# Kernel tuning notes

Hardware: AMD Instinct MI355X
Metric: run time of the kernel (lower is better)

Reference implementation:

```python
import jax, jax.numpy as jnp
from jax import lax
import numpy as np

CONF_THRES = 0.25
IOU_THRES = 0.45
MAX_WH = 7680.0   # per-class box offset (yolov5 agnostic=False trick)
TOP_K = 5000      # pre-NMS candidate cap (yolov5 uses max_nms=30000; capped for tractable IoU matrix)


def _xywh2xyxy(b):
    xy, wh = b[..., :2], b[..., 2:4]
    half = wh * 0.5
    return jnp.concatenate([xy - half, xy + half], axis=-1)


def _box_iou(a, b):
    # a: [K,4], b: [K,4] xyxy -> [K,K]
    area_a = (a[:, 2] - a[:, 0]) * (a[:, 3] - a[:, 1])
    area_b = (b[:, 2] - b[:, 0]) * (b[:, 3] - b[:, 1])
    lt = jnp.maximum(a[:, None, :2], b[None, :, :2])
    rb = jnp.minimum(a[:, None, 2:], b[None, :, 2:])
    wh = jnp.clip(rb - lt, 0.0)
    inter = wh[..., 0] * wh[..., 1]
    return inter / (area_a[:, None] + area_b[None, :] - inter + 1e-7)


def _nms_single(pred_i, max_det):
    # pred_i: [N, 5+nc] = (x, y, w, h, obj, cls...)
    obj = pred_i[:, 4]
    cls_conf = pred_i[:, 5:] * obj[:, None]          # conf = obj * cls
    score = jnp.max(cls_conf, axis=-1)                # best class (multi_label=False)
    cls = jnp.argmax(cls_conf, axis=-1).astype(pred_i.dtype)
    boxes = _xywh2xyxy(pred_i[:, :4])
    valid = (obj > CONF_THRES) & (score > CONF_THRES)
    mscore = jnp.where(valid, score, -1.0)

    # pre-NMS top-k candidates by confidence (yolov5 sorts by conf)
    top_s, idx = lax.top_k(mscore, TOP_K)
    tb = boxes[idx]                                   # [K,4]
    tc = cls[idx]                                     # [K]
    tvalid = top_s > 0.0

    # offset boxes by class so different classes never suppress each other
    ob = tb + (tc * MAX_WH)[:, None]
    iou = lax.stop_gradient(_box_iou(ob, ob))         # [K,K]
    ar = jnp.arange(TOP_K)

    def step(keep, i):
        sup = keep[i] & (iou[i] > IOU_THRES) & (ar > i)
        return keep & ~sup, None

    keep, _ = lax.scan(step, tvalid, ar)
    keep = keep & tvalid

    fscore = jnp.where(keep, top_s, -1.0)
    fs, fi = lax.top_k(fscore, max_det)
    det = jnp.concatenate([tb[fi], top_s[fi][:, None], tc[fi][:, None]], axis=-1)  # [max_det, 6]
    return jnp.where((fs > 0.0)[:, None], det, 0.0)


def setup_inputs() -> dict:
    key = jax.random.key(0)
    k1, k2, k3, k4 = jax.random.split(key, 4)
    B, N, NC = 8, 25200, 80
    xy = jax.random.uniform(k1, (B, N, 2)) * 608.0 + 16.0
    wh = jax.random.uniform(k2, (B, N, 2)) * 120.0 + 8.0
    obj = jax.random.uniform(k3, (B, N, 1))
    cls = jax.random.uniform(k4, (B, N, NC))
    pred = jnp.concatenate([xy, wh, obj, cls], axis=-1).astype(jnp.float32)
    return {"pred": pred, "max_det": 300}


def reference(pred, max_det):
    # pred: [B, N, 5+nc] -> detections [B, max_det, 6] = (x1, y1, x2, y2, conf, cls)
    return jax.vmap(lambda p: _nms_single(p, max_det))(pred)
```

## Files before the change

kernel.cpp:

```cpp
#include <hip/hip_runtime.h>

typedef unsigned long long ull;

#define N_PRED 25200
#define NCLS   80
#define ROWW   85
#define TOPK   5000
#define IOU_T  0.45f
#define MAXWH  7680.0f

#define K2T    1024
#define MAXE   25
#define CAP    512
#define CAPB   256
#define PTPB   256
#define PROWS  128
#define K4T    1024
#define MAXE4  5
#define SELN   320

__device__ __forceinline__ int SIX(int d) { return d + (d >> 5); }

__device__ __forceinline__ void scan_find(const unsigned* hist, int nb, unsigned k, ull* sbd) {
  const int l = (int)threadIdx.x;
  const int bpl = nb >> 6;
  unsigned s = 0;
  for (int j = 0; j < bpl; ++j) s += hist[SIX(l * bpl + j)];
  unsigned suf = s;
  #pragma unroll
  for (int o = 1; o < 64; o <<= 1) {
    unsigned t = __shfl_down(suf, (unsigned)o, 64);
    if (l + o < 64) suf += t;
  }
  unsigned sufN = __shfl_down(suf, 1u, 64);
  if (l == 63) sufN = 0;
  if (suf >= k && sufN < k) {
    unsigned cum = sufN;
    for (int j = bpl - 1; j >= 0; --j) {
      unsigned c = hist[SIX(l * bpl + j)];
      if (cum + c >= k) { sbd[0] = (ull)(l * bpl + j); sbd[1] = (ull)(k - cum); break; }
      cum += c;
    }
  }
}

__global__ __launch_bounds__(1024) void zero_kernel(unsigned* __restrict__ z, int nwords) {
  int i = blockIdx.x * 1024 + (int)threadIdx.x;
  if (i < nwords) z[i] = 0u;
}

__global__ __launch_bounds__(PTPB) void prep_kernel(const float* __restrict__ pred,
    ull* __restrict__ pk, unsigned char* __restrict__ cls8, unsigned* __restrict__ ghist) {
  __shared__ float sr[PROWS * ROWW];
  __shared__ unsigned hist[2048];
  const int b = blockIdx.y;
  const int rbase = blockIdx.x * PROWS;
  int nrows = N_PRED - rbase; if (nrows > PROWS) nrows = PROWS;
  const int tid = (int)threadIdx.x;
  for (int i = tid; i < 2048; i += PTPB) hist[i] = 0;
  const float* src = pred + ((size_t)b * N_PRED + rbase) * ROWW;
  const int nfl4 = (nrows * ROWW) >> 2;
  for (int i = tid; i < nfl4; i += PTPB) {
    float4 t; __builtin_memcpy(&t, src + i * 4, 16);
    *(float4*)&sr[i * 4] = t;
  }
  __syncthreads();
  const int r = tid >> 1, h = tid & 1;
  if (r < nrows) {
    const float* row = sr + r * ROWW;
    float obj = row[4];
    float best = -1.0f; int bi = 0;
    const int c0 = h * 40;
    for (int c = 0; c < 40; ++c) {
      float p = __fmul_rn(row[5 + c0 + c], obj);
      if (p > best) { best = p; bi = c0 + c; }
    }
    float ob_ = __shfl_xor(best, 1, 64);
    int   oi  = __shfl_xor(bi, 1, 64);
    if (h == 0) {
      if (!(best >= ob_)) { best = ob_; bi = oi; }
      bool valid = (obj > 0.25f) && (best > 0.25f);
      float ms = valid ? best : -1.0f;
      unsigned kb = __float_as_uint(ms);
      kb = (kb & 0x80000000u) ? ~kb : (kb | 0x80000000u);
      const int g = rbase + r;
      pk[(size_t)b * N_PRED + g] = ((ull)kb << 32) | (unsigned)~(unsigned)g;
      cls8[(size_t)b * N_PRED + g] = (unsigned char)bi;
      atomicAdd(&hist[kb >> 21], 1u);
    }
  }
  __syncthreads();
  for (int i = tid; i < 2048; i += PTPB) {
    unsigned cn = hist[i];
    if (cn) atomicAdd(&ghist[b * 2048 + i], cn);
  }
}

__global__ __launch_bounds__(K2T) void thresh_kernel(const ull* __restrict__ pkArr,
    const unsigned* __restrict__ ghist, const unsigned char* __restrict__ cls8,
    ull* __restrict__ bucket, unsigned* __restrict__ bucketCnt) {
  __shared__ unsigned hist[2112];
  __shared__ ull sbd[2];
  const int b = blockIdx.x;
  const int tid = (int)threadIdx.x;
  ull v[MAXE];
  #pragma unroll
  for (int e = 0; e < MAXE; ++e) {
    int i = tid + e * K2T;
    v[e] = (i < N_PRED) ? pkArr[(size_t)b * N_PRED + i] : 0ull;
  }
  unsigned k = TOPK;
  ull pfx = 0;
  for (int i = tid; i < 2048; i += K2T) hist[SIX(i)] = ghist[b * 2048 + i];
  __syncthreads();
  if (tid < 64) scan_find(hist, 2048, k, sbd);
  __syncthreads();
  {
    ull d = sbd[0]; unsigned kp = (unsigned)sbd[1];
    unsigned c = hist[SIX((int)d)];
    pfx |= d << 53; k = kp;
    if (kp != c) {
      const int shifts[5] = {42, 31, 20, 9, 0};
      const int widths[5] = {11, 11, 11, 11, 9};
      for (int p = 0; p < 5; ++p) {
        const int sh = shifts[p];
        const int nb = 1 << widths[p];
        __syncthreads();
        for (int i = tid; i < 2112; i += K2T) hist[i] = 0;
        __syncthreads();
        const int hb = sh + widths[p];
        const ull hm = ~((1ull << hb) - 1ull);
        #pragma unroll
        for (int e = 0; e < MAXE; ++e) {
          ull pv = v[e];
          if ((pv & hm) == pfx)
            atomicAdd(&hist[SIX((int)((pv >> sh) & (ull)(nb - 1)))], 1u);
        }
        __syncthreads();
        if (tid < 64) scan_find(hist, nb, k, sbd);
        __syncthreads();
        ull d2 = sbd[0]; unsigned kp2 = (unsigned)sbd[1];
        unsigned c2 = hist[SIX((int)d2)];
        pfx |= d2 << sh; k = kp2;
        if (kp2 == c2) break;
      }
    }
  }
  const ull thr = pfx;
  #pragma unroll
  for (int e = 0; e < MAXE; ++e) {
    ull pv = v[e];
    if (pv >= thr && (pv >> 63)) {
      unsigned idx = ~(unsigned)(pv & 0xFFFFFFFFull);
      int c = (int)cls8[(size_t)b * N_PRED + idx];
      unsigned pos = atomicAdd(&bucketCnt[b * NCLS + c], 1u);
      if (pos < CAP) bucket[((size_t)b * NCLS + c) * CAP + pos] = pv;
    }
  }
}

__global__ __launch_bounds__(64) void nms_kernel(const ull* __restrict__ bucket,
    const unsigned* __restrict__ bucketCnt, const float* __restrict__ pred,
    ull* __restrict__ keptPk, float4* __restrict__ keptBox, float2* __restrict__ keptSC,
    unsigned* __restrict__ keptCnt) {
  const int c = blockIdx.x, b = blockIdx.y, lane = (int)threadIdx.x;
  __shared__ ull su[CAPB];
  __shared__ ull spk[CAPB];
  __shared__ float4 sob[CAPB];
  __shared__ float4 srb[CAPB];
  unsigned kxu = bucketCnt[b * NCLS + c];
  int kx = (kxu > CAPB) ? CAPB : (int)kxu;
  if (kx == 0) return;
  const float cf = (float)c;
  const float off = __fmul_rn(cf, MAXWH);
  const ull* bk = bucket + ((size_t)b * NCLS + c) * CAP;
  for (int i = lane; i < kx; i += 64) su[i] = bk[i];
  __syncthreads();
  {
    ull mine[4]; int rk[4] = {0, 0, 0, 0};
    #pragma unroll
    for (int r = 0; r < 4; ++r) mine[r] = (r * 64 + lane < kx) ? su[r * 64 + lane] : 0ull;
    for (int j = 0; j < kx; ++j) {
      ull x = su[j];
      #pragma unroll
      for (int r = 0; r < 4; ++r) rk[r] += (x > mine[r]) ? 1 : 0;
    }
    #pragma unroll
    for (int r = 0; r < 4; ++r)
      if (r * 64 + lane < kx) spk[rk[r]] = mine[r];
  }
  __syncthreads();
  for (int i = lane; i < kx; i += 64) {
    unsigned idx = ~(unsigned)(spk[i] & 0xFFFFFFFFull);
    float4 t0; __builtin_memcpy(&t0, pred + ((size_t)b * N_PRED + idx) * ROWW, 16);
    float hw = __fmul_rn(t0.z, 0.5f), hh = __fmul_rn(t0.w, 0.5f);
    float4 rb = make_float4(__fsub_rn(t0.x, hw), __fsub_rn(t0.y, hh),
                            __fadd_rn(t0.x, hw), __fadd_rn(t0.y, hh));
    srb[i] = rb;
    sob[i] = make_float4(__fadd_rn(rb.x, off), __fadd_rn(rb.y, off),
                         __fadd_rn(rb.z, off), __fadd_rn(rb.w, off));
  }
  __syncthreads();
  ull rowm[4][4] = {{0ull}};
  #pragma unroll
  for (int r = 0; r < 4; ++r) {
    if (r * 64 < kx) {
      const int i = r * 64 + lane;
      const bool act = i < kx;
      float4 A = sob[act ? i : 0];
      float areaA = __fmul_rn(__fsub_rn(A.z, A.x), __fsub_rn(A.w, A.y));
      #pragma unroll
      for (int w = 0; w < 4; ++w) {
        if (w >= r && w * 64 < kx) {
          ull m = 0ull;
          int jmax = kx - w * 64; if (jmax > 64) jmax = 64;
          for (int jj = 0; jj < jmax; ++jj) {
            const int j = w * 64 + jj;
            float4 Bx = sob[j];
            float areaB = __fmul_rn(__fsub_rn(Bx.z, Bx.x), __fsub_rn(Bx.w, Bx.y));
            float wx = fmaxf(__fsub_rn(fminf(A.z, Bx.z), fmaxf(A.x, Bx.x)), 0.0f);
            float wy = fmaxf(__fsub_rn(fminf(A.w, Bx.w), fmaxf(A.y, Bx.y)), 0.0f);
            float inter = __fmul_rn(wx, wy);
            float denom = __fadd_rn(__fsub_rn(__fadd_rn(areaA, areaB), inter), 1e-7f);
            float iou = __fdiv_rn(inter, denom);
            if (act && j > i && iou > IOU_T) m |= 1ull << jj;
          }
          rowm[r][w] = m;
        }
      }
    }
  }
  ull alive[4];
  #pragma unroll
  for (int w = 0; w < 4; ++w) {
    int rem = kx - w * 64;
    alive[w] = (rem >= 64) ? ~0ull : (rem > 0 ? ((1ull << rem) - 1ull) : 0ull);
  }
  #pragma unroll
  for (int w = 0; w < 4; ++w) {
    if (w * 64 < kx) {
      int bmax = kx - w * 64; if (bmax > 64) bmax = 64;
      for (int bit = 0; bit < bmax; ++bit) {
        if ((alive[w] >> bit) & 1ull) {
          #pragma unroll
          for (int w2 = 0; w2 < 4; ++w2) {
            if (w2 >= w && w2 * 64 < kx) {
              ull row = __shfl(rowm[w][w2], bit, 64);
              alive[w2] &= ~row;
            }
          }
        }
      }
    }
  }
  int tot = 0;
  #pragma unroll
  for (int w = 0; w < 4; ++w) tot += (int)__popcll(alive[w]);
  unsigned gbase = 0;
  if (lane == 0) gbase = atomicAdd(&keptCnt[b], (unsigned)tot);
  gbase = __shfl(gbase, 0, 64);
  unsigned pre = 0;
  #pragma unroll
  for (int w = 0; w < 4; ++w) {
    if (w * 64 < kx) {
      ull aw = alive[w];
      int i = w * 64 + lane;
      bool kp = (i < kx) && ((aw >> lane) & 1ull);
      if (kp) {
        unsigned pos = gbase + pre + (unsigned)__popcll(aw & ((1ull << lane) - 1ull));
        if (pos < TOPK) {
          ull p = spk[i];
          keptPk[(size_t)b * TOPK + pos] = p;
          keptBox[(size_t)b * TOPK + pos] = srb[i];
          keptSC[(size_t)b * TOPK + pos] =
              make_float2(__uint_as_float((unsigned)(p >> 32) & 0x7FFFFFFFu), cf);
        }
      }
      pre += (unsigned)__popcll(aw);
    }
  }
}

__global__ __launch_bounds__(K4T) void out_kernel(const ull* __restrict__ keptPk,
    const float4* __restrict__ keptBox, const float2* __restrict__ keptSC,
    const unsigned* __restrict__ keptCnt, float* __restrict__ out, int maxdet) {
  __shared__ unsigned hist[2112];
  __shared__ ull sbd[2];
  __shared__ ull sPk[SELN];
  __shared__ int sSlot[SELN];
  __shared__ unsigned scnt;
  const int b = blockIdx.x;
  const int tid = (int)threadIdx.x;
  float* ob = out + (size_t)b * maxdet * 6;
  const unsigned K = keptCnt[b];
  const unsigned kk = (K < (unsigned)maxdet) ? K : (unsigned)maxdet;
  for (int i = (int)kk * 6 + tid; i < maxdet * 6; i += K4T) ob[i] = 0.0f;
  if (kk == 0) return;
  ull v[MAXE4];
  #pragma unroll
  for (int e = 0; e < MAXE4; ++e) {
    unsigned i = (unsigned)tid + e * K4T;
    v[e] = (i < K) ? keptPk[(size_t)b * TOPK + i] : 0ull;
  }
  ull thr = 1ull;
  if (K > (unsigned)maxdet) {
    unsigned k = kk;
    ull pfx = 0;
    const int shifts[6] = {53, 42, 31, 20, 9, 0};
    const int widths[6] = {11, 11, 11, 11, 11, 9};
    for (int p = 0; p < 6; ++p) {
      const int sh = shifts[p];
      const int nb = 1 << widths[p];
      for (int i = tid; i < 2112; i += K4T) hist[i] = 0;
      __syncthreads();
      const int hb = sh + widths[p];
      const ull hm = (hb >= 64) ? 0ull : ~((1ull << hb) - 1ull);
      #pragma unroll
      for (int e = 0; e < MAXE4; ++e) {
        ull pv = v[e];
        if (pv != 0ull && (pv & hm) == pfx)
          atomicAdd(&hist[SIX((int)((pv >> sh) & (ull)(nb - 1)))], 1u);
      }
      __syncthreads();
      if (tid < 64) scan_find(hist, nb, k, sbd);
      __syncthreads();
      ull d = sbd[0]; unsigned kp = (unsigned)sbd[1];
      unsigned c = hist[SIX((int)d)];
      pfx |= d << sh; k = kp;
      if (kp == c) break;
      __syncthreads();
    }
    thr = pfx;
  }
  if (tid == 0) scnt = 0;
  __syncthreads();
  const int lane = tid & 63;
  #pragma unroll
  for (int e = 0; e < MAXE4; ++e) {
    unsigned i = (unsigned)tid + e * K4T;
    bool sel = (i < K) && (v[e] >= thr);
    ull m = __ballot(sel);
    if (m) {
      unsigned basep = 0;
      if (lane == 0) basep = atomicAdd(&scnt, (unsigned)__popcll(m));
      basep = __shfl(basep, 0, 64);
      if (sel) {
        unsigned pos = basep + (unsigned)__popcll(m & ((1ull << lane) - 1ull));
        if (pos < SELN) { sPk[pos] = v[e]; sSlot[pos] = (int)i; }
      }
    }
  }
  __syncthreads();
  const int n = (int)scnt;
  for (int i = tid; i < n; i += K4T) {
    ull mypk = sPk[i];
    int rank = 0;
    for (int j = 0; j < n; ++j) rank += (sPk[j] > mypk) ? 1 : 0;
    if (rank < maxdet) {
      int slot = sSlot[i];
      float4 bx = keptBox[(size_t)b * TOPK + slot];
      float2 sc = keptSC[(size_t)b * TOPK + slot];
      float* dst = ob + (size_t)rank * 6;
      dst[0] = bx.x; dst[1] = bx.y; dst[2] = bx.z; dst[3] = bx.w;
      dst[4] = sc.x; dst[5] = sc.y;
    }
  }
}

extern "C" void kernel_launch(void* const* d_in, const int* in_sizes, int n_in,
                              void* d_out, int out_size, void* d_ws, size_t ws_size,
                              hipStream_t stream) {
  const float* pred = (const float*)d_in[0];
  const int B = in_sizes[0] / (N_PRED * ROWW);
  const int maxdet = out_size / (B * 6);

  char* p = (char*)d_ws;
  auto carve = [&](size_t bytes) { char* r = p; p += (bytes + 255) & ~(size_t)255; return (void*)r; };
  ull*           pk   = (ull*)carve((size_t)B * N_PRED * 8);
  unsigned char* cls8 = (unsigned char*)carve((size_t)B * N_PRED);
  size_t zbytes = (size_t)B * 2048 * 4 + (size_t)B * NCLS * 4 + (size_t)B * 4;
  char*     zbase     = (char*)carve(zbytes);
  unsigned* ghist     = (unsigned*)zbase;
  unsigned* bucketCnt = (unsigned*)(zbase + (size_t)B * 2048 * 4);
  unsigned* keptCnt   = (unsigned*)(zbase + (size_t)B * 2048 * 4 + (size_t)B * NCLS * 4);
  ull*      bucket  = (ull*)carve((size_t)B * NCLS * CAP * 8);
  ull*      keptPk  = (ull*)carve((size_t)B * TOPK * 8);
  float4*   keptBox = (float4*)carve((size_t)B * TOPK * 16);
  float2*   keptSC  = (float2*)carve((size_t)B * TOPK * 8);

  const int nwords = (int)(zbytes / 4);
  zero_kernel<<<(nwords + 1023) / 1024, 1024, 0, stream>>>((unsigned*)zbase, nwords);
  prep_kernel<<<dim3((N_PRED + PROWS - 1) / PROWS, B), PTPB, 0, stream>>>(pred, pk, cls8, ghist);
  thresh_kernel<<<B, K2T, 0, stream>>>(pk, ghist, cls8, bucket, bucketCnt);
  nms_kernel<<<dim3(NCLS, B), 64, 0, stream>>>(bucket, bucketCnt, pred,
                                               keptPk, keptBox, keptSC, keptCnt);
  out_kernel<<<B, K4T, 0, stream>>>(keptPk, keptBox, keptSC, keptCnt, (float*)d_out, maxdet);
}
```

Before: 111.9 us.

## Fuse threshold, per-class NMS and output selection into one per-batch kernel

Merges the threshold/bucketing, per-class NMS and final top-k output kernels into a single 1024-thread block per batch. Each wavefront handles classes in turn, with the per-class bucket cap reduced to 128. The prep kernel now processes one row per loop step across a whole wavefront, reading the row directly from global memory and reducing the class max with shuffles instead of staging rows in LDS. This removes two launches and global counter traffic. The cost is that NMS parallelism drops from 640 blocks to 8 blocks of 16 wavefronts, and the smaller cap risks dropping candidates in large classes.

```diff
diff --git a/kernel.cpp b/kernel.cpp
--- a/kernel.cpp
+++ b/kernel.cpp
@@ -9,13 +9,9 @@
 #define IOU_T  0.45f
 #define MAXWH  7680.0f
 
-#define K2T    1024
 #define MAXE   25
-#define CAP    512
-#define CAPB   256
-#define PTPB   256
-#define PROWS  128
-#define K4T    1024
+#define CAP    128
+#define PRPB   256
 #define MAXE4  5
 #define SELN   320
 
@@ -49,69 +45,79 @@
   if (i < nwords) z[i] = 0u;
 }
 
-__global__ __launch_bounds__(PTPB) void prep_kernel(const float* __restrict__ pred,
+__global__ __launch_bounds__(256) void prep_kernel(const float* __restrict__ pred,
     ull* __restrict__ pk, unsigned char* __restrict__ cls8, unsigned* __restrict__ ghist) {
-  __shared__ float sr[PROWS * ROWW];
   __shared__ unsigned hist[2048];
   const int b = blockIdx.y;
-  const int rbase = blockIdx.x * PROWS;
-  int nrows = N_PRED - rbase; if (nrows > PROWS) nrows = PROWS;
-  const int tid = (int)threadIdx.x;
-  for (int i = tid; i < 2048; i += PTPB) hist[i] = 0;
-  const float* src = pred + ((size_t)b * N_PRED + rbase) * ROWW;
-  const int nfl4 = (nrows * ROWW) >> 2;
-  for (int i = tid; i < nfl4; i += PTPB) {
-    float4 t; __builtin_memcpy(&t, src + i * 4, 16);
-    *(float4*)&sr[i * 4] = t;
-  }
-  __syncthreads();
-  const int r = tid >> 1, h = tid & 1;
-  if (r < nrows) {
-    const float* row = sr + r * ROWW;
+  const int tid = (int)threadIdx.x, lane = tid & 63, wv = tid >> 6;
+  for (int i = tid; i < 2048; i += 256) hist[i] = 0;
+  __syncthreads();
+  const int rbase = blockIdx.x * PRPB + wv * 64;
+  int rows = N_PRED - rbase; if (rows > 64) rows = 64;
+  ull mypk = 0; int mycls = 0, mybin = 0;
+  #pragma unroll 4
+  for (int t = 0; t < rows; ++t) {
+    const float* row = pred + ((size_t)b * N_PRED + (rbase + t)) * ROWW;
     float obj = row[4];
-    float best = -1.0f; int bi = 0;
-    const int c0 = h * 40;
-    for (int c = 0; c < 40; ++c) {
-      float p = __fmul_rn(row[5 + c0 + c], obj);
-      if (p > best) { best = p; bi = c0 + c; }
-    }
-    float ob_ = __shfl_xor(best, 1, 64);
-    int   oi  = __shfl_xor(bi, 1, 64);
-    if (h == 0) {
-      if (!(best >= ob_)) { best = ob_; bi = oi; }
+    float best = __fmul_rn(row[5 + lane], obj);
+    int bi = lane;
+    if (lane < 16) {
+      float p2 = __fmul_rn(row[69 + lane], obj);
+      if (p2 > best) { best = p2; bi = 64 + lane; }
+    }
+    #pragma unroll
+    for (int m = 32; m; m >>= 1) {
+      float ob = __shfl_xor(best, m, 64);
+      int   oi = __shfl_xor(bi, m, 64);
+      if (ob > best || (ob == best && oi < bi)) { best = ob; bi = oi; }
+    }
+    if (lane == t) {
       bool valid = (obj > 0.25f) && (best > 0.25f);
       float ms = valid ? best : -1.0f;
       unsigned kb = __float_as_uint(ms);
       kb = (kb & 0x80000000u) ? ~kb : (kb | 0x80000000u);
-      const int g = rbase + r;
-      pk[(size_t)b * N_PRED + g] = ((ull)kb << 32) | (unsigned)~(unsigned)g;
-      cls8[(size_t)b * N_PRED + g] = (unsigned char)bi;
-      atomicAdd(&hist[kb >> 21], 1u);
-    }
-  }
-  __syncthreads();
-  for (int i = tid; i < 2048; i += PTPB) {
+      mypk = ((ull)kb << 32) | (unsigned)~(unsigned)(rbase + t);
+      mycls = bi; mybin = (int)(kb >> 21);
+    }
+  }
+  if (lane < rows) {
+    const int g = rbase + lane;
+    pk[(size_t)b * N_PRED + g] = mypk;
+    cls8[(size_t)b * N_PRED + g] = (unsigned char)mycls;
+    atomicAdd(&hist[mybin], 1u);
+  }
+  __syncthreads();
+  for (int i = tid; i < 2048; i += 256) {
     unsigned cn = hist[i];
     if (cn) atomicAdd(&ghist[b * 2048 + i], cn);
   }
 }
 
-__global__ __launch_bounds__(K2T) void thresh_kernel(const ull* __restrict__ pkArr,
+__global__ __launch_bounds__(1024) void snms_kernel(const ull* __restrict__ pkArr,
     const unsigned* __restrict__ ghist, const unsigned char* __restrict__ cls8,
-    ull* __restrict__ bucket, unsigned* __restrict__ bucketCnt) {
+    const float* __restrict__ pred, ull* __restrict__ bucket,
+    ull* __restrict__ keptPk, float4* __restrict__ keptBox, float2* __restrict__ keptSC,
+    float* __restrict__ out, int maxdet) {
   __shared__ unsigned hist[2112];
   __shared__ ull sbd[2];
+  __shared__ unsigned bCnt[NCLS];
+  __shared__ unsigned keptCnt;
+  __shared__ unsigned scnt;
+  __shared__ ull wscr[16 * 384];
   const int b = blockIdx.x;
-  const int tid = (int)threadIdx.x;
+  const int tid = (int)threadIdx.x, lane = tid & 63, wv = tid >> 6;
+
+  if (tid < NCLS) bCnt[tid] = 0;
+  if (tid == 0) { keptCnt = 0; scnt = 0; }
   ull v[MAXE];
   #pragma unroll
   for (int e = 0; e < MAXE; ++e) {
-    int i = tid + e * K2T;
+    int i = tid + e * 1024;
     v[e] = (i < N_PRED) ? pkArr[(size_t)b * N_PRED + i] : 0ull;
   }
   unsigned k = TOPK;
   ull pfx = 0;
-  for (int i = tid; i < 2048; i += K2T) hist[SIX(i)] = ghist[b * 2048 + i];
+  for (int i = tid; i < 2048; i += 1024) hist[SIX(i)] = ghist[b * 2048 + i];
   __syncthreads();
   if (tid < 64) scan_find(hist, 2048, k, sbd);
   __syncthreads();
@@ -126,7 +132,7 @@
         const int sh = shifts[p];
         const int nb = 1 << widths[p];
         __syncthreads();
-        for (int i = tid; i < 2112; i += K2T) hist[i] = 0;
+        for (int i = tid; i < 2112; i += 1024) hist[i] = 0;
         __syncthreads();
         const int hb = sh + widths[p];
         const ull hm = ~((1ull << hb) - 1ull);
@@ -153,192 +159,176 @@
     if (pv >= thr && (pv >> 63)) {
       unsigned idx = ~(unsigned)(pv & 0xFFFFFFFFull);
       int c = (int)cls8[(size_t)b * N_PRED + idx];
-      unsigned pos = atomicAdd(&bucketCnt[b * NCLS + c], 1u);
+      unsigned pos = atomicAdd(&bCnt[c], 1u);
       if (pos < CAP) bucket[((size_t)b * NCLS + c) * CAP + pos] = pv;
     }
   }
-}
-
-__global__ __launch_bounds__(64) void nms_kernel(const ull* __restrict__ bucket,
-    const unsigned* __restrict__ bucketCnt, const float* __restrict__ pred,
-    ull* __restrict__ keptPk, float4* __restrict__ keptBox, float2* __restrict__ keptSC,
-    unsigned* __restrict__ keptCnt) {
-  const int c = blockIdx.x, b = blockIdx.y, lane = (int)threadIdx.x;
-  __shared__ ull su[CAPB];
-  __shared__ ull spk[CAPB];
-  __shared__ float4 sob[CAPB];
-  __shared__ float4 srb[CAPB];
-  unsigned kxu = bucketCnt[b * NCLS + c];
-  int kx = (kxu > CAPB) ? CAPB : (int)kxu;
-  if (kx == 0) return;
-  const float cf = (float)c;
-  const float off = __fmul_rn(cf, MAXWH);
-  const ull* bk = bucket + ((size_t)b * NCLS + c) * CAP;
-  for (int i = lane; i < kx; i += 64) su[i] = bk[i];
-  __syncthreads();
-  {
-    ull mine[4]; int rk[4] = {0, 0, 0, 0};
-    #pragma unroll
-    for (int r = 0; r < 4; ++r) mine[r] = (r * 64 + lane < kx) ? su[r * 64 + lane] : 0ull;
-    for (int j = 0; j < kx; ++j) {
-      ull x = su[j];
-      #pragma unroll
-      for (int r = 0; r < 4; ++r) rk[r] += (x > mine[r]) ? 1 : 0;
-    }
-    #pragma unroll
-    for (int r = 0; r < 4; ++r)
-      if (r * 64 + lane < kx) spk[rk[r]] = mine[r];
-  }
-  __syncthreads();
-  for (int i = lane; i < kx; i += 64) {
-    unsigned idx = ~(unsigned)(spk[i] & 0xFFFFFFFFull);
-    float4 t0; __builtin_memcpy(&t0, pred + ((size_t)b * N_PRED + idx) * ROWW, 16);
-    float hw = __fmul_rn(t0.z, 0.5f), hh = __fmul_rn(t0.w, 0.5f);
-    float4 rb = make_float4(__fsub_rn(t0.x, hw), __fsub_rn(t0.y, hh),
-                            __fadd_rn(t0.x, hw), __fadd_rn(t0.y, hh));
-    srb[i] = rb;
-    sob[i] = make_float4(__fadd_rn(rb.x, off), __fadd_rn(rb.y, off),
-                         __fadd_rn(rb.z, off), __fadd_rn(rb.w, off));
-  }
-  __syncthreads();
-  ull rowm[4][4] = {{0ull}};
-  #pragma unroll
-  for (int r = 0; r < 4; ++r) {
-    if (r * 64 < kx) {
-      const int i = r * 64 + lane;
-      const bool act = i < kx;
-      float4 A = sob[act ? i : 0];
-      float areaA = __fmul_rn(__fsub_rn(A.z, A.x), __fsub_rn(A.w, A.y));
-      #pragma unroll
-      for (int w = 0; w < 4; ++w) {
-        if (w >= r && w * 64 < kx) {
-          ull m = 0ull;
-          int jmax = kx - w * 64; if (jmax > 64) jmax = 64;
-          for (int jj = 0; jj < jmax; ++jj) {
-            const int j = w * 64 + jj;
-            float4 Bx = sob[j];
-            float areaB = __fmul_rn(__fsub_rn(Bx.z, Bx.x), __fsub_rn(Bx.w, Bx.y));
-            float wx = fmaxf(__fsub_rn(fminf(A.z, Bx.z), fmaxf(A.x, Bx.x)), 0.0f);
-            float wy = fmaxf(__fsub_rn(fminf(A.w, Bx.w), fmaxf(A.y, Bx.y)), 0.0f);
-            float inter = __fmul_rn(wx, wy);
-            float denom = __fadd_rn(__fsub_rn(__fadd_rn(areaA, areaB), inter), 1e-7f);
-            float iou = __fdiv_rn(inter, denom);
-            if (act && j > i && iou > IOU_T) m |= 1ull << jj;
-          }
-          rowm[r][w] = m;
+  __syncthreads();
+
+  ull* skey = wscr + (size_t)wv * 384;
+  float4* sow = (float4*)(skey + 128);
+  for (int cc = wv; cc < NCLS; cc += 16) {
+    unsigned kxu = bCnt[cc];
+    int kx = (kxu > (unsigned)CAP) ? CAP : (int)kxu;
+    if (kx == 0) continue;
+    const float cf = (float)cc;
+    const float off = __fmul_rn(cf, MAXWH);
+    const ull* bk = bucket + ((size_t)b * NCLS + cc) * CAP;
+    if (lane < kx) skey[lane] = bk[lane];
+    if (64 + lane < kx) skey[64 + lane] = bk[64 + lane];
+    ull m0 = (lane < kx) ? skey[lane] : 0ull;
+    ull m1 = (64 + lane < kx) ? skey[64 + lane] : 0ull;
+    int r0 = 0, r1 = 0;
+    for (int j = 0; j < kx; ++j) { ull x = skey[j]; r0 += (x > m0) ? 1 : 0; r1 += (x > m1) ? 1 : 0; }
+    if (lane < kx) skey[r0] = m0;
+    if (64 + lane < kx) skey[r1] = m1;
+    ull pk0 = 0, pk1 = 0;
+    float4 rb0 = make_float4(0,0,0,0), rb1 = rb0, ob0 = rb0, ob1 = rb0;
+    if (lane < kx) {
+      pk0 = skey[lane];
+      unsigned idx = ~(unsigned)(pk0 & 0xFFFFFFFFull);
+      float4 t0; __builtin_memcpy(&t0, pred + ((size_t)b * N_PRED + idx) * ROWW, 16);
+      float hw = __fmul_rn(t0.z, 0.5f), hh = __fmul_rn(t0.w, 0.5f);
+      rb0 = make_float4(__fsub_rn(t0.x, hw), __fsub_rn(t0.y, hh),
+                        __fadd_rn(t0.x, hw), __fadd_rn(t0.y, hh));
+      ob0 = make_float4(__fadd_rn(rb0.x, off), __fadd_rn(rb0.y, off),
+                        __fadd_rn(rb0.z, off), __fadd_rn(rb0.w, off));
+      sow[lane] = ob0;
+    }
+    if (64 + lane < kx) {
+      pk1 = skey[64 + lane];
+      unsigned idx = ~(unsigned)(pk1 & 0xFFFFFFFFull);
+      float4 t0; __builtin_memcpy(&t0, pred + ((size_t)b * N_PRED + idx) * ROWW, 16);
+      float hw = __fmul_rn(t0.z, 0.5f), hh = __fmul_rn(t0.w, 0.5f);
+      rb1 = make_float4(__fsub_rn(t0.x, hw), __fsub_rn(t0.y, hh),
+                        __fadd_rn(t0.x, hw), __fadd_rn(t0.y, hh));
+      ob1 = make_float4(__fadd_rn(rb1.x, off), __fadd_rn(rb1.y, off),
+                        __fadd_rn(rb1.z, off), __fadd_rn(rb1.w, off));
+      sow[64 + lane] = ob1;
+    }
+    ull rm00 = 0ull, rm01 = 0ull, rm11 = 0ull;
+    {
+      const bool a0 = lane < kx;
+      float area0 = __fmul_rn(__fsub_rn(ob0.z, ob0.x), __fsub_rn(ob0.w, ob0.y));
+      int jm = kx < 64 ? kx : 64;
+      for (int jj = 0; jj < jm; ++jj) {
+        float4 Bx = sow[jj];
+        float areaB = __fmul_rn(__fsub_rn(Bx.z, Bx.x), __fsub_rn(Bx.w, Bx.y));
+        float wx = fmaxf(__fsub_rn(fminf(ob0.z, Bx.z), fmaxf(ob0.x, Bx.x)), 0.0f);
+        float wy = fmaxf(__fsub_rn(fminf(ob0.w, Bx.w), fmaxf(ob0.y, Bx.y)), 0.0f);
+        float inter = __fmul_rn(wx, wy);
+        float denom = __fadd_rn(__fsub_rn(__fadd_rn(area0, areaB), inter), 1e-7f);
+        if (a0 && jj > lane && __fdiv_rn(inter, denom) > IOU_T) rm00 |= 1ull << jj;
+      }
+      if (kx > 64) {
+        const bool a1 = 64 + lane < kx;
+        float area1 = __fmul_rn(__fsub_rn(ob1.z, ob1.x), __fsub_rn(ob1.w, ob1.y));
+        int jm1 = kx - 64;
+        for (int jj = 0; jj < jm1; ++jj) {
+          float4 Bx = sow[64 + jj];
+          float areaB = __fmul_rn(__fsub_rn(Bx.z, Bx.x), __fsub_rn(Bx.w, Bx.y));
+          float wx = fmaxf(__fsub_rn(fminf(ob0.z, Bx.z), fmaxf(ob0.x, Bx.x)), 0.0f);
+          float wy = fmaxf(__fsub_rn(fminf(ob0.w, Bx.w), fmaxf(ob0.y, Bx.y)), 0.0f);
+          float inter = __fmul_rn(wx, wy);
+          float denom = __fadd_rn(__fsub_rn(__fadd_rn(area0, areaB), inter), 1e-7f);
+          if (a0 && __fdiv_rn(inter, denom) > IOU_T) rm01 |= 1ull << jj;
+          float wx1 = fmaxf(__fsub_rn(fminf(ob1.z, Bx.z), fmaxf(ob1.x, Bx.x)), 0.0f);
+          float wy1 = fmaxf(__fsub_rn(fminf(ob1.w, Bx.w), fmaxf(ob1.y, Bx.y)), 0.0f);
+          float inter1 = __fmul_rn(wx1, wy1);
+          float denom1 = __fadd_rn(__fsub_rn(__fadd_rn(area1, areaB), inter1), 1e-7f);
+          if (a1 && jj > lane && __fdiv_rn(inter1, denom1) > IOU_T) rm11 |= 1ull << jj;
         }
       }
     }
-  }
-  ull alive[4];
-  #pragma unroll
-  for (int w = 0; w < 4; ++w) {
-    int rem = kx - w * 64;
-    alive[w] = (rem >= 64) ? ~0ull : (rem > 0 ? ((1ull << rem) - 1ull) : 0ull);
-  }
-  #pragma unroll
-  for (int w = 0; w < 4; ++w) {
-    if (w * 64 < kx) {
-      int bmax = kx - w * 64; if (bmax > 64) bmax = 64;
-      for (int bit = 0; bit < bmax; ++bit) {
-        if ((alive[w] >> bit) & 1ull) {
-          #pragma unroll
-          for (int w2 = 0; w2 < 4; ++w2) {
-            if (w2 >= w && w2 * 64 < kx) {
-              ull row = __shfl(rowm[w][w2], bit, 64);
-              alive[w2] &= ~row;
-            }
-          }
+    ull alive0 = (kx >= 64) ? ~0ull : ((1ull << kx) - 1ull);
+    ull alive1 = (kx > 64) ? (((kx - 64) >= 64) ? ~0ull : ((1ull << (kx - 64)) - 1ull)) : 0ull;
+    {
+      int bm = kx < 64 ? kx : 64;
+      for (int bit = 0; bit < bm; ++bit) {
+        if ((alive0 >> bit) & 1ull) {
+          alive0 &= ~__shfl(rm00, bit, 64);
+          if (kx > 64) alive1 &= ~__shfl(rm01, bit, 64);
         }
       }
-    }
-  }
-  int tot = 0;
-  #pragma unroll
-  for (int w = 0; w < 4; ++w) tot += (int)__popcll(alive[w]);
-  unsigned gbase = 0;
-  if (lane == 0) gbase = atomicAdd(&keptCnt[b], (unsigned)tot);
-  gbase = __shfl(gbase, 0, 64);
-  unsigned pre = 0;
-  #pragma unroll
-  for (int w = 0; w < 4; ++w) {
-    if (w * 64 < kx) {
-      ull aw = alive[w];
-      int i = w * 64 + lane;
-      bool kp = (i < kx) && ((aw >> lane) & 1ull);
-      if (kp) {
-        unsigned pos = gbase + pre + (unsigned)__popcll(aw & ((1ull << lane) - 1ull));
-        if (pos < TOPK) {
-          ull p = spk[i];
-          keptPk[(size_t)b * TOPK + pos] = p;
-          keptBox[(size_t)b * TOPK + pos] = srb[i];
-          keptSC[(size_t)b * TOPK + pos] =
-              make_float2(__uint_as_float((unsigned)(p >> 32) & 0x7FFFFFFFu), cf);
-        }
-      }
-      pre += (unsigned)__popcll(aw);
-    }
-  }
-}
-
-__global__ __launch_bounds__(K4T) void out_kernel(const ull* __restrict__ keptPk,
-    const float4* __restrict__ keptBox, const float2* __restrict__ keptSC,
-    const unsigned* __restrict__ keptCnt, float* __restrict__ out, int maxdet) {
-  __shared__ unsigned hist[2112];
-  __shared__ ull sbd[2];
-  __shared__ ull sPk[SELN];
-  __shared__ int sSlot[SELN];
-  __shared__ unsigned scnt;
-  const int b = blockIdx.x;
-  const int tid = (int)threadIdx.x;
+      if (kx > 64) {
+        int bm1 = kx - 64;
+        for (int bit = 0; bit < bm1; ++bit)
+          if ((alive1 >> bit) & 1ull) alive1 &= ~__shfl(rm11, bit, 64);
+      }
+    }
+    int tot = (int)__popcll(alive0) + (int)__popcll(alive1);
+    unsigned gbase = 0;
+    if (lane == 0) gbase = atomicAdd(&keptCnt, (unsigned)tot);
+    gbase = __shfl(gbase, 0, 64);
+    const ull below = (1ull << lane) - 1ull;
+    if ((lane < kx) && ((alive0 >> lane) & 1ull)) {
+      unsigned pos = gbase + (unsigned)__popcll(alive0 & below);
+      if (pos < TOPK) {
+        keptPk[(size_t)b * TOPK + pos] = pk0;
+        keptBox[(size_t)b * TOPK + pos] = rb0;
+        keptSC[(size_t)b * TOPK + pos] =
+            make_float2(__uint_as_float((unsigned)(pk0 >> 32) & 0x7FFFFFFFu), cf);
+      }
+    }
+    if ((64 + lane < kx) && ((alive1 >> lane) & 1ull)) {
+      unsigned pos = gbase + (unsigned)__popcll(alive0) + (unsigned)__popcll(alive1 & below);
+      if (pos < TOPK) {
+        keptPk[(size_t)b * TOPK + pos] = pk1;
+        keptBox[(size_t)b * TOPK + pos] = rb1;
+        keptSC[(size_t)b * TOPK + pos] =
+            make_float2(__uint_as_float((unsigned)(pk1 >> 32) & 0x7FFFFFFFu), cf);
+      }
+    }
+  }
+  __syncthreads();
+
+  ull* sPk = wscr;
+  int* sSlot = (int*)(wscr + SELN);
   float* ob = out + (size_t)b * maxdet * 6;
-  const unsigned K = keptCnt[b];
+  const unsigned K = keptCnt;
   const unsigned kk = (K < (unsigned)maxdet) ? K : (unsigned)maxdet;
-  for (int i = (int)kk * 6 + tid; i < maxdet * 6; i += K4T) ob[i] = 0.0f;
+  for (int i = (int)kk * 6 + tid; i < maxdet * 6; i += 1024) ob[i] = 0.0f;
   if (kk == 0) return;
-  ull v[MAXE4];
+  ull v2[MAXE4];
   #pragma unroll
   for (int e = 0; e < MAXE4; ++e) {
-    unsigned i = (unsigned)tid + e * K4T;
-    v[e] = (i < K) ? keptPk[(size_t)b * TOPK + i] : 0ull;
-  }
-  ull thr = 1ull;
+    unsigned i = (unsigned)tid + e * 1024;
+    v2[e] = (i < K) ? keptPk[(size_t)b * TOPK + i] : 0ull;
+  }
+  ull thr2 = 1ull;
   if (K > (unsigned)maxdet) {
-    unsigned k = kk;
-    ull pfx = 0;
+    unsigned k2 = kk;
+    ull pfx2 = 0;
     const int shifts[6] = {53, 42, 31, 20, 9, 0};
     const int widths[6] = {11, 11, 11, 11, 11, 9};
     for (int p = 0; p < 6; ++p) {
       const int sh = shifts[p];
       const int nb = 1 << widths[p];
-      for (int i = tid; i < 2112; i += K4T) hist[i] = 0;
+      for (int i = tid; i < 2112; i += 1024) hist[i] = 0;
       __syncthreads();
       const int hb = sh + widths[p];
       const ull hm = (hb >= 64) ? 0ull : ~((1ull << hb) - 1ull);
       #pragma unroll
       for (int e = 0; e < MAXE4; ++e) {
-        ull pv = v[e];
-        if (pv != 0ull && (pv & hm) == pfx)
+        ull pv = v2[e];
+        if (pv != 0ull && (pv & hm) == pfx2)
           atomicAdd(&hist[SIX((int)((pv >> sh) & (ull)(nb - 1)))], 1u);
       }
       __syncthreads();
-      if (tid < 64) scan_find(hist, nb, k, sbd);
+      if (tid < 64) scan_find(hist, nb, k2, sbd);
       __syncthreads();
       ull d = sbd[0]; unsigned kp = (unsigned)sbd[1];
       unsigned c = hist[SIX((int)d)];
-      pfx |= d << sh; k = kp;
+      pfx2 |= d << sh; k2 = kp;
       if (kp == c) break;
       __syncthreads();
     }
-    thr = pfx;
-  }
-  if (tid == 0) scnt = 0;
-  __syncthreads();
-  const int lane = tid & 63;
+    thr2 = pfx2;
+  }
   #pragma unroll
   for (int e = 0; e < MAXE4; ++e) {
-    unsigned i = (unsigned)tid + e * K4T;
-    bool sel = (i < K) && (v[e] >= thr);
+    unsigned i = (unsigned)tid + e * 1024;
+    bool sel = (i < K) && (v2[e] >= thr2);
     ull m = __ballot(sel);
     if (m) {
       unsigned basep = 0;
@@ -346,13 +336,13 @@
       basep = __shfl(basep, 0, 64);
       if (sel) {
         unsigned pos = basep + (unsigned)__popcll(m & ((1ull << lane) - 1ull));
-        if (pos < SELN) { sPk[pos] = v[e]; sSlot[pos] = (int)i; }
+        if (pos < SELN) { sPk[pos] = v2[e]; sSlot[pos] = (int)i; }
       }
     }
   }
   __syncthreads();
   const int n = (int)scnt;
-  for (int i = tid; i < n; i += K4T) {
+  for (int i = tid; i < n; i += 1024) {
     ull mypk = sPk[i];
     int rank = 0;
     for (int j = 0; j < n; ++j) rank += (sPk[j] > mypk) ? 1 : 0;
@@ -376,23 +366,17 @@
 
   char* p = (char*)d_ws;
   auto carve = [&](size_t bytes) { char* r = p; p += (bytes + 255) & ~(size_t)255; return (void*)r; };
-  ull*           pk   = (ull*)carve((size_t)B * N_PRED * 8);
-  unsigned char* cls8 = (unsigned char*)carve((size_t)B * N_PRED);
-  size_t zbytes = (size_t)B * 2048 * 4 + (size_t)B * NCLS * 4 + (size_t)B * 4;
-  char*     zbase     = (char*)carve(zbytes);
-  unsigned* ghist     = (unsigned*)zbase;
-  unsigned* bucketCnt = (unsigned*)(zbase + (size_t)B * 2048 * 4);
-  unsigned* keptCnt   = (unsigned*)(zbase + (size_t)B * 2048 * 4 + (size_t)B * NCLS * 4);
+  ull*           pk    = (ull*)carve((size_t)B * N_PRED * 8);
+  unsigned char* cls8  = (unsigned char*)carve((size_t)B * N_PRED);
+  unsigned*      ghist = (unsigned*)carve((size_t)B * 2048 * 4);
   ull*      bucket  = (ull*)carve((size_t)B * NCLS * CAP * 8);
   ull*      keptPk  = (ull*)carve((size_t)B * TOPK * 8);
   float4*   keptBox = (float4*)carve((size_t)B * TOPK * 16);
   float2*   keptSC  = (float2*)carve((size_t)B * TOPK * 8);
 
-  const int nwords = (int)(zbytes / 4);
-  zero_kernel<<<(nwords + 1023) / 1024, 1024, 0, stream>>>((unsigned*)zbase, nwords);
-  prep_kernel<<<dim3((N_PRED + PROWS - 1) / PROWS, B), PTPB, 0, stream>>>(pred, pk, cls8, ghist);
-  thresh_kernel<<<B, K2T, 0, stream>>>(pk, ghist, cls8, bucket, bucketCnt);
-  nms_kernel<<<dim3(NCLS, B), 64, 0, stream>>>(bucket, bucketCnt, pred,
-                                               keptPk, keptBox, keptSC, keptCnt);
-  out_kernel<<<B, K4T, 0, stream>>>(keptPk, keptBox, keptSC, keptCnt, (float*)d_out, maxdet);
-}
+  const int nwords = B * 2048;
+  zero_kernel<<<(nwords + 1023) / 1024, 1024, 0, stream>>>(ghist, nwords);
+  prep_kernel<<<dim3((N_PRED + PRPB - 1) / PRPB, B), 256, 0, stream>>>(pred, pk, cls8, ghist);
+  snms_kernel<<<B, 1024, 0, stream>>>(pk, ghist, cls8, pred, bucket,
+                                      keptPk, keptBox, keptSC, (float*)d_out, maxdet);
+}
```

Result: slower. 265.5 us (+137.3%).

## Drop zero kernel and global histogram; build top-bits histogram in thresh kernel

Applied to the files above, without the earlier changes.

Removes the separate zeroing kernel and the per-block shared/global histogram atomics in prep_kernel. The first-pass 11-bit histogram is now built inside thresh_kernel from the values it already holds in registers, and bucketCnt/keptCnt are zeroed there too. This saves one kernel launch and the global atomics. In exchange, the histogram work moves into the thresh kernel, which runs only B=8 blocks and adds 25 shared atomics per thread.

```diff
diff --git a/kernel.cpp b/kernel.cpp
--- a/kernel.cpp
+++ b/kernel.cpp
@@ -44,20 +44,13 @@
   }
 }
 
-__global__ __launch_bounds__(1024) void zero_kernel(unsigned* __restrict__ z, int nwords) {
-  int i = blockIdx.x * 1024 + (int)threadIdx.x;
-  if (i < nwords) z[i] = 0u;
-}
-
 __global__ __launch_bounds__(PTPB) void prep_kernel(const float* __restrict__ pred,
-    ull* __restrict__ pk, unsigned char* __restrict__ cls8, unsigned* __restrict__ ghist) {
+    ull* __restrict__ pk, unsigned char* __restrict__ cls8) {
   __shared__ float sr[PROWS * ROWW];
-  __shared__ unsigned hist[2048];
   const int b = blockIdx.y;
   const int rbase = blockIdx.x * PROWS;
   int nrows = N_PRED - rbase; if (nrows > PROWS) nrows = PROWS;
   const int tid = (int)threadIdx.x;
-  for (int i = tid; i < 2048; i += PTPB) hist[i] = 0;
   const float* src = pred + ((size_t)b * N_PRED + rbase) * ROWW;
   const int nfl4 = (nrows * ROWW) >> 2;
   for (int i = tid; i < nfl4; i += PTPB) {
@@ -86,33 +79,33 @@
       const int g = rbase + r;
       pk[(size_t)b * N_PRED + g] = ((ull)kb << 32) | (unsigned)~(unsigned)g;
       cls8[(size_t)b * N_PRED + g] = (unsigned char)bi;
-      atomicAdd(&hist[kb >> 21], 1u);
-    }
-  }
-  __syncthreads();
-  for (int i = tid; i < 2048; i += PTPB) {
-    unsigned cn = hist[i];
-    if (cn) atomicAdd(&ghist[b * 2048 + i], cn);
+    }
   }
 }
 
 __global__ __launch_bounds__(K2T) void thresh_kernel(const ull* __restrict__ pkArr,
-    const unsigned* __restrict__ ghist, const unsigned char* __restrict__ cls8,
-    ull* __restrict__ bucket, unsigned* __restrict__ bucketCnt) {
+    const unsigned char* __restrict__ cls8, ull* __restrict__ bucket,
+    unsigned* __restrict__ bucketCnt, unsigned* __restrict__ keptCnt) {
   __shared__ unsigned hist[2112];
   __shared__ ull sbd[2];
   const int b = blockIdx.x;
   const int tid = (int)threadIdx.x;
+  if (tid < NCLS) bucketCnt[b * NCLS + tid] = 0;
+  if (tid == 0) keptCnt[b] = 0;
   ull v[MAXE];
   #pragma unroll
   for (int e = 0; e < MAXE; ++e) {
     int i = tid + e * K2T;
     v[e] = (i < N_PRED) ? pkArr[(size_t)b * N_PRED + i] : 0ull;
   }
+  for (int i = tid; i < 2112; i += K2T) hist[i] = 0;
+  __syncthreads();
+  #pragma unroll
+  for (int e = 0; e < MAXE; ++e)
+    atomicAdd(&hist[SIX((int)(v[e] >> 53))], 1u);
+  __syncthreads();
   unsigned k = TOPK;
   ull pfx = 0;
-  for (int i = tid; i < 2048; i += K2T) hist[SIX(i)] = ghist[b * 2048 + i];
-  __syncthreads();
   if (tid < 64) scan_find(hist, 2048, k, sbd);
   __syncthreads();
   {
@@ -376,22 +369,17 @@
 
   char* p = (char*)d_ws;
   auto carve = [&](size_t bytes) { char* r = p; p += (bytes + 255) & ~(size_t)255; return (void*)r; };
-  ull*           pk   = (ull*)carve((size_t)B * N_PRED * 8);
-  unsigned char* cls8 = (unsigned char*)carve((size_t)B * N_PRED);
-  size_t zbytes = (size_t)B * 2048 * 4 + (size_t)B * NCLS * 4 + (size_t)B * 4;
-  char*     zbase     = (char*)carve(zbytes);
-  unsigned* ghist     = (unsigned*)zbase;
-  unsigned* bucketCnt = (unsigned*)(zbase + (size_t)B * 2048 * 4);
-  unsigned* keptCnt   = (unsigned*)(zbase + (size_t)B * 2048 * 4 + (size_t)B * NCLS * 4);
+  ull*           pk       = (ull*)carve((size_t)B * N_PRED * 8);
+  unsigned char* cls8     = (unsigned char*)carve((size_t)B * N_PRED);
+  unsigned*      bucketCnt= (unsigned*)carve((size_t)B * NCLS * 4);
+  unsigned*      keptCnt  = (unsigned*)carve((size_t)B * 4);
   ull*      bucket  = (ull*)carve((size_t)B * NCLS * CAP * 8);
   ull*      keptPk  = (ull*)carve((size_t)B * TOPK * 8);
   float4*   keptBox = (float4*)carve((size_t)B * TOPK * 16);
   float2*   keptSC  = (float2*)carve((size_t)B * TOPK * 8);
 
-  const int nwords = (int)(zbytes / 4);
-  zero_kernel<<<(nwords + 1023) / 1024, 1024, 0, stream>>>((unsigned*)zbase, nwords);
-  prep_kernel<<<dim3((N_PRED + PROWS - 1) / PROWS, B), PTPB, 0, stream>>>(pred, pk, cls8, ghist);
-  thresh_kernel<<<B, K2T, 0, stream>>>(pk, ghist, cls8, bucket, bucketCnt);
+  prep_kernel<<<dim3((N_PRED + PROWS - 1) / PROWS, B), PTPB, 0, stream>>>(pred, pk, cls8);
+  thresh_kernel<<<B, K2T, 0, stream>>>(pk, cls8, bucket, bucketCnt, keptCnt);
   nms_kernel<<<dim3(NCLS, B), 64, 0, stream>>>(bucket, bucketCnt, pred,
                                                keptPk, keptBox, keptSC, keptCnt);
   out_kernel<<<B, K4T, 0, stream>>>(keptPk, keptBox, keptSC, keptCnt, (float*)d_out, maxdet);
```

Result: faster. 109.5 us (-2.2%).
